# Performance work log

Measured on AMD Instinct MI355X. Metric: run time of the kernel, lower is better.

## Reference

```python
import jax, jax.numpy as jnp
import numpy as np

_BN_EPS = 1e-5
_BN_SCALE = 1.0 / np.sqrt(1.0 + _BN_EPS)  # eval-mode BN with running_mean=0, running_var=1


def _bn(x, g, b):
    # eval-mode BatchNorm1d over channel dim (last axis here)
    return x * (g * _BN_SCALE) + b


def _sa_layer(src_xyz, dst_xyz, cur_i, idx, empty, p_w, p_g, p_b, m_w, m_g, m_b):
    # src_xyz: (N,3), dst_xyz: (M,3), cur_i: (N,D), idx: (M,S) int, empty: (M,) bool
    idx = idx.astype(jnp.int32)
    sp = src_xyz[idx]                       # (M,S,3) neighbor gather
    dp = dst_xyz[:, None, :]                # (M,1,3)
    feat6 = jnp.concatenate([sp - dp, jnp.broadcast_to(dp, sp.shape)], axis=-1)  # (M,S,6)
    off = jax.nn.silu(_bn(jnp.einsum('msc,dc->msd', feat6, p_w), p_g, p_b))      # (M,S,D)
    x = off + cur_i[idx]                    # (M,S,D)
    x = jnp.where(empty[:, None, None], 0.0, x)
    h = jax.nn.relu(_bn(jnp.einsum('msd,hd->msh', x, m_w), m_g, m_b))            # (M,S,H)
    return jnp.max(h, axis=1)               # (M,H) max-pool over neighbors


def reference(src_xyz, src_feats, dst_xyz, idx0, idx1, empty0, empty1,
              fc0_w, fc0_b, p0_w, p0_g, p0_b, m0_w, m0_g, m0_b,
              fc1_w, fc1_b, p1_w, p1_g, p1_b, m1_w, m1_g, m1_b,
              out_w, out_g, out_b):
    cur0 = src_feats @ fc0_w.T + fc0_b      # (N,64) fc_i of layer 0
    cur1 = src_feats @ fc1_w.T + fc1_b      # (N,64) fc_i of layer 1
    f0 = _sa_layer(src_xyz, dst_xyz, cur0, idx0, empty0, p0_w, p0_g, p0_b, m0_w, m0_g, m0_b)
    f1 = _sa_layer(src_xyz, dst_xyz, cur1, idx1, empty1, p1_w, p1_g, p1_b, m1_w, m1_g, m1_b)
    feats = jnp.concatenate([f0, f1], axis=1)                                    # (M,256)
    out = jax.nn.relu(_bn(feats @ out_w.T, out_g, out_b))                        # out_conv (1x1 conv)
    return out                               # (M,256)


def setup_inputs() -> dict:
    key = jax.random.key(0)
    ks = jax.random.split(key, 24)
    N, M, Cin, D, H, S0, S1 = 65536, 16384, 64, 64, 128, 16, 32
    inp = {
        'src_xyz': jax.random.normal(ks[0], (N, 3), jnp.float32) * 20.0,
        'src_feats': jax.random.normal(ks[1], (N, Cin), jnp.float32),
        'dst_xyz': jax.random.normal(ks[2], (M, 3), jnp.float32) * 20.0,
        'idx0': jax.random.randint(ks[3], (M, S0), 0, N, jnp.int32),
        'idx1': jax.random.randint(ks[4], (M, S1), 0, N, jnp.int32),
        'empty0': jax.random.bernoulli(ks[5], 0.05, (M,)),
        'empty1': jax.random.bernoulli(ks[6], 0.05, (M,)),
        'fc0_w': jax.random.normal(ks[7], (D, Cin), jnp.float32) / np.sqrt(Cin),
        'fc0_b': jnp.zeros((D,), jnp.float32),
        'p0_w': jax.random.normal(ks[8], (D, 6), jnp.float32) / np.sqrt(6.0),
        'p0_g': jnp.ones((D,), jnp.float32),
        'p0_b': jnp.zeros((D,), jnp.float32),
        'm0_w': jax.random.normal(ks[9], (H, D), jnp.float32) / np.sqrt(D),
        'm0_g': jnp.ones((H,), jnp.float32),
        'm0_b': jnp.zeros((H,), jnp.float32),
        'fc1_w': jax.random.normal(ks[10], (D, Cin), jnp.float32) / np.sqrt(Cin),
        'fc1_b': jnp.zeros((D,), jnp.float32),
        'p1_w': jax.random.normal(ks[11], (D, 6), jnp.float32) / np.sqrt(6.0),
        'p1_g': jnp.ones((D,), jnp.float32),
        'p1_b': jnp.zeros((D,), jnp.float32),
        'm1_w': jax.random.normal(ks[12], (H, D), jnp.float32) / np.sqrt(D),
        'm1_g': jnp.ones((H,), jnp.float32),
        'm1_b': jnp.zeros((H,), jnp.float32),
        'out_w': jax.random.normal(ks[13], (256, 2 * H), jnp.float32) / np.sqrt(2.0 * H),
        'out_g': jnp.ones((256,), jnp.float32),
        'out_b': jnp.zeros((256,), jnp.float32),
    }
    return inp
```

## Files before the change

### kernel.cpp

```cpp
#include <hip/hip_runtime.h>
#include <hip/hip_bf16.h>

typedef unsigned short ushort_t;
typedef unsigned int uint_t;
typedef __attribute__((ext_vector_type(8))) short v8s;
typedef __attribute__((ext_vector_type(4))) float v4f;

#define BN_SCALE 0.9999950000374997f

__device__ __forceinline__ float bf2f(ushort_t u) {
    union { uint_t i; float f; } v;
    v.i = ((uint_t)u) << 16;
    return v.f;
}
__device__ __forceinline__ ushort_t f2bf(float f) {
    union { uint_t i; float f; } v;
    v.f = f;
    uint_t b = v.i;
    b += 0x7fffu + ((b >> 16) & 1u);
    return (ushort_t)(b >> 16);
}

__device__ __forceinline__ v8s cvt8(const float* __restrict__ p) {
    v8s f;
    #pragma unroll
    for (int j = 0; j < 8; ++j) f[j] = (short)f2bf(p[j]);
    return f;
}

__global__ __launch_bounds__(256) void cur_conv_kernel(
    const float* __restrict__ src_feats,
    const float* __restrict__ fc0_w, const float* __restrict__ fc0_b,
    const float* __restrict__ fc1_w, const float* __restrict__ fc1_b,
    ushort_t* __restrict__ cur0, ushort_t* __restrict__ cur1,
    const float* __restrict__ out_w, ushort_t* __restrict__ out_wb,
    const float* __restrict__ m0_w,  ushort_t* __restrict__ m0_wb,
    const float* __restrict__ m1_w,  ushort_t* __restrict__ m1_wb,
    const int CURB)
{
    if (blockIdx.x >= CURB) {
        const int b = blockIdx.x - CURB;
        const float* src;
        ushort_t* dst;
        int base;
        if (b < 64)      { src = out_w; dst = out_wb; base = b; }
        else if (b < 72) { src = m0_w;  dst = m0_wb;  base = b - 64; }
        else             { src = m1_w;  dst = m1_wb;  base = b - 72; }
        const int i = (base * 256 + threadIdx.x) * 4;
        const v4f v = *(const v4f*)(src + i);
        ushort_t r0 = f2bf(v[0]), r1 = f2bf(v[1]), r2 = f2bf(v[2]), r3 = f2bf(v[3]);
        uint_t lo = (uint_t)r0 | ((uint_t)r1 << 16);
        uint_t hi = (uint_t)r2 | ((uint_t)r3 << 16);
        *(uint2*)(dst + i) = make_uint2(lo, hi);
        return;
    }

    const int tid  = threadIdx.x;
    const int lane = tid & 63;
    const int wid  = tid >> 6;
    const int col  = lane & 15;
    const int quad = lane >> 4;
    const int row0 = blockIdx.x * 64 + wid * 16;

    v8s afrag[2];
    #pragma unroll
    for (int kf = 0; kf < 2; ++kf)
        afrag[kf] = cvt8(src_feats + (size_t)(row0 + col) * 64 + kf * 32 + quad * 8);

    v4f acc[8];
    v8s bfrag[8][2];
    #pragma unroll
    for (int ct = 0; ct < 8; ++ct) {
        const int d = (ct & 3) * 16 + col;
        const float* w = (ct < 4 ? fc0_w : fc1_w) + d * 64;
        const float  b = (ct < 4 ? fc0_b : fc1_b)[d];
        acc[ct] = (v4f){b, b, b, b};
        #pragma unroll
        for (int kf = 0; kf < 2; ++kf)
            bfrag[ct][kf] = cvt8(w + kf * 32 + quad * 8);
    }

    #pragma unroll
    for (int kf = 0; kf < 2; ++kf)
        #pragma unroll
        for (int ct = 0; ct < 8; ++ct)
            acc[ct] = __builtin_amdgcn_mfma_f32_16x16x32_bf16(
                afrag[kf], bfrag[ct][kf], acc[ct], 0, 0, 0);

    #pragma unroll
    for (int ct = 0; ct < 8; ++ct) {
        ushort_t* dst = (ct < 4) ? cur0 : cur1;
        const int d = (ct & 3) * 16 + col;
        #pragma unroll
        for (int r = 0; r < 4; ++r) {
            const int n = row0 + quad * 4 + r;
            dst[(size_t)n * 64 + d] = f2bf(acc[ct][r]);
        }
    }
}

template <int S>
__device__ __forceinline__ void sa_body(
    const int bid,
    const float* __restrict__ src_xyz,
    const float* __restrict__ dst_xyz,
    const int*   __restrict__ idx,
    const int*   __restrict__ empty,
    const float* __restrict__ p_w,
    const float* __restrict__ p_g,
    const float* __restrict__ p_b,
    const ushort_t* __restrict__ m_wb,
    const float* __restrict__ m_g,
    const float* __restrict__ m_b,
    const ushort_t* __restrict__ cur,
    ushort_t*    __restrict__ f01,
    const int layer_off,
    ushort_t* xlds,
    v4f*      flds)
{
    constexpr int PAIRS = 128;
    constexpr int MB = PAIRS / S;
    constexpr int XP = 72;
    constexpr int T  = S / 4;

    const int tid  = threadIdx.x;
    const int lane = tid & 63;
    const int wid  = tid >> 6;
    const int m0   = bid * MB;

    {
        const int p  = tid >> 1;
        const int hf = tid & 1;
        const int m  = m0 + p / S;
        const int i  = idx[(size_t)m * S + (p & (S - 1))];
        const uint_t* crow = (const uint_t*)(cur + (size_t)i * 64) + hf * 16;
        const uint4 c0 = *(const uint4*)(crow + 0);
        const uint4 c1 = *(const uint4*)(crow + 4);
        const uint4 c2 = *(const uint4*)(crow + 8);
        const uint4 c3 = *(const uint4*)(crow + 12);
        uint_t* drow = (uint_t*)(xlds + p * XP) + hf * 16;
        *(uint4*)(drow + 0)  = c0;
        *(uint4*)(drow + 4)  = c1;
        *(uint4*)(drow + 8)  = c2;
        *(uint4*)(drow + 12) = c3;
    }
    if (tid < PAIRS) {
        const int p = tid;
        const int m = m0 + p / S;
        const int i = idx[(size_t)m * S + (p & (S - 1))];
        const float dx = dst_xyz[m * 3 + 0];
        const float dy = dst_xyz[m * 3 + 1];
        const float dz = dst_xyz[m * 3 + 2];
        v4f r;
        r[0] = src_xyz[i * 3 + 0] - dx;
        r[1] = src_xyz[i * 3 + 1] - dy;
        r[2] = src_xyz[i * 3 + 2] - dz;
        r[3] = 0.0f;
        flds[p] = r;
    }

    const int dd = (lane & 31) * 2;
    const int psub = lane >> 5;
    const float pgA = p_g[dd] * BN_SCALE;
    const float pgB = p_g[dd + 1] * BN_SCALE;
    const float pbA = p_b[dd];
    const float pbB = p_b[dd + 1];
    const float pwA0 = p_w[dd * 6 + 0] * pgA;
    const float pwA1 = p_w[dd * 6 + 1] * pgA;
    const float pwA2 = p_w[dd * 6 + 2] * pgA;
    const float pdA0 = p_w[dd * 6 + 3] * pgA;
    const float pdA1 = p_w[dd * 6 + 4] * pgA;
    const float pdA2 = p_w[dd * 6 + 5] * pgA;
    const float pwB0 = p_w[dd * 6 + 6] * pgB;
    const float pwB1 = p_w[dd * 6 + 7] * pgB;
    const float pwB2 = p_w[dd * 6 + 8] * pgB;
    const float pdB0 = p_w[dd * 6 + 9] * pgB;
    const float pdB1 = p_w[dd * 6 + 10] * pgB;
    const float pdB2 = p_w[dd * 6 + 11] * pgB;

    __syncthreads();

    const int tbase = wid * T;
    #pragma unroll
    for (int mi = 0; mi < MB; ++mi) {
        const int m = m0 + mi;
        const float dx = dst_xyz[m * 3 + 0];
        const float dy = dst_xyz[m * 3 + 1];
        const float dz = dst_xyz[m * 3 + 2];
        const int   em = empty[m];
        const float vbA = fmaf(pdA0, dx, fmaf(pdA1, dy, fmaf(pdA2, dz, pbA)));
        const float vbB = fmaf(pdB0, dx, fmaf(pdB1, dy, fmaf(pdB2, dz, pbB)));

        #pragma unroll
        for (int it = 0; it < T / 2; ++it) {
            const int p = mi * S + tbase + it * 2 + psub;
            const v4f r = flds[p];
            const uint_t cu = *(const uint_t*)(xlds + p * XP + dd);
            const float c0 = __uint_as_float(cu << 16);
            const float c1 = __uint_as_float(cu & 0xffff0000u);

            const float v0 = fmaf(pwA0, r[0], fmaf(pwA1, r[1], fmaf(pwA2, r[2], vbA)));
            const float v1 = fmaf(pwB0, r[0], fmaf(pwB1, r[1], fmaf(pwB2, r[2], vbB)));
            const float rc0 = __builtin_amdgcn_rcpf(1.0f + __expf(-v0));
            const float rc1 = __builtin_amdgcn_rcpf(1.0f + __expf(-v1));
            float x0 = fmaf(v0, rc0, c0);
            float x1 = fmaf(v1, rc1, c1);
            x0 = em ? 0.0f : x0;
            x1 = em ? 0.0f : x1;

            float2 f2; f2.x = x0; f2.y = x1;
            union { __hip_bfloat162 h2; uint_t u; } pk;
            pk.h2 = __float22bfloat162_rn(f2);
            *(uint_t*)(xlds + p * XP + dd) = pk.u;
        }
    }

    const int col  = lane & 15;
    const int quad = lane >> 4;
    v8s bfrag[2][2];
    float mgv[2], mbv[2];
    #pragma unroll
    for (int c = 0; c < 2; ++c) {
        const int h = (wid * 2 + c) * 16 + col;
        #pragma unroll
        for (int kf = 0; kf < 2; ++kf)
            bfrag[c][kf] = *(const v8s*)(m_wb + h * 64 + kf * 32 + quad * 8);
        mgv[c] = m_g[h] * BN_SCALE;
        mbv[c] = m_b[h];
    }

    __syncthreads();

    #pragma unroll
    for (int mi = 0; mi < MB; ++mi) {
        const int m = m0 + mi;
        v4f acc[S / 16][2];
        #pragma unroll
        for (int rt = 0; rt < S / 16; ++rt)
            #pragma unroll
            for (int c = 0; c < 2; ++c)
                acc[rt][c] = (v4f)0.0f;

        #pragma unroll
        for (int rt = 0; rt < S / 16; ++rt) {
            #pragma unroll
            for (int kf = 0; kf < 2; ++kf) {
                const v8s afrag = *(const v8s*)(
                    xlds + ((mi * S + rt * 16 + col)) * XP + kf * 32 + quad * 8);
                acc[rt][0] = __builtin_amdgcn_mfma_f32_16x16x32_bf16(
                    afrag, bfrag[0][kf], acc[rt][0], 0, 0, 0);
                acc[rt][1] = __builtin_amdgcn_mfma_f32_16x16x32_bf16(
                    afrag, bfrag[1][kf], acc[rt][1], 0, 0, 0);
            }
        }

        float vmax0 = 0.0f, vmax1 = 0.0f;
        #pragma unroll
        for (int c = 0; c < 2; ++c) {
            float vm = 0.0f;
            #pragma unroll
            for (int rt = 0; rt < S / 16; ++rt)
                #pragma unroll
                for (int r = 0; r < 4; ++r) {
                    const float y = fmaf(acc[rt][c][r], mgv[c], mbv[c]);
                    vm = fmaxf(vm, y);
                }
            vm = fmaxf(vm, __shfl_xor(vm, 16));
            vm = fmaxf(vm, __shfl_xor(vm, 32));
            if (c == 0) vmax0 = vm; else vmax1 = vm;
        }
        if (lane < 32) {
            const int c = lane >> 4;
            const float val = (c == 0) ? vmax0 : vmax1;
            f01[m * 256 + layer_off + (wid * 2 + c) * 16 + (lane & 15)] = f2bf(val);
        }
    }
}

__global__ __launch_bounds__(256, 6) void sa_fused_kernel(
    const float* __restrict__ src_xyz, const float* __restrict__ dst_xyz,
    const int* __restrict__ idx0, const int* __restrict__ empty0,
    const float* __restrict__ p0_w, const float* __restrict__ p0_g, const float* __restrict__ p0_b,
    const ushort_t* __restrict__ m0_wb, const float* __restrict__ m0_g, const float* __restrict__ m0_b,
    const ushort_t* __restrict__ cur0,
    const int* __restrict__ idx1, const int* __restrict__ empty1,
    const float* __restrict__ p1_w, const float* __restrict__ p1_g, const float* __restrict__ p1_b,
    const ushort_t* __restrict__ m1_wb, const float* __restrict__ m1_g, const float* __restrict__ m1_b,
    const ushort_t* __restrict__ cur1,
    ushort_t* __restrict__ f01, const int G32)
{
    __shared__ __align__(16) ushort_t xlds[128 * 72];
    __shared__ v4f      flds[128];

    const int b = blockIdx.x;
    if (b < G32)
        sa_body<32>(b, src_xyz, dst_xyz, idx1, empty1, p1_w, p1_g, p1_b,
                    m1_wb, m1_g, m1_b, cur1, f01, 128, xlds, flds);
    else
        sa_body<16>(b - G32, src_xyz, dst_xyz, idx0, empty0, p0_w, p0_g, p0_b,
                    m0_wb, m0_g, m0_b, cur0, f01, 0, xlds, flds);
}

__global__ __launch_bounds__(256) void out_kernel(
    const ushort_t* __restrict__ f01,
    const ushort_t* __restrict__ out_wb,
    const float*    __restrict__ out_g,
    const float*    __restrict__ out_b,
    float*          __restrict__ out)
{
    const int tid  = threadIdx.x;
    const int lane = tid & 63;
    const int wid  = tid >> 6;
    const int col  = lane & 15;
    const int quad = lane >> 4;
    const int m0   = blockIdx.x * 16;

    v8s afrag[8];
    #pragma unroll
    for (int kf = 0; kf < 8; ++kf)
        afrag[kf] = *(const v8s*)(f01 + (size_t)(m0 + col) * 256 + kf * 32 + quad * 8);

    v4f acc[4];
    #pragma unroll
    for (int c = 0; c < 4; ++c) acc[c] = (v4f)0.0f;

    #pragma unroll
    for (int kf = 0; kf < 8; ++kf) {
        #pragma unroll
        for (int c = 0; c < 4; ++c) {
            const int n = (wid * 4 + c) * 16 + col;
            const v8s b = *(const v8s*)(out_wb + (size_t)n * 256 + kf * 32 + quad * 8);
            acc[c] = __builtin_amdgcn_mfma_f32_16x16x32_bf16(afrag[kf], b, acc[c], 0, 0, 0);
        }
    }

    #pragma unroll
    for (int c = 0; c < 4; ++c) {
        const int n  = (wid * 4 + c) * 16 + col;
        const float og = out_g[n] * BN_SCALE;
        const float ob = out_b[n];
        #pragma unroll
        for (int r = 0; r < 4; ++r) {
            float y = fmaf(acc[c][r], og, ob);
            y = fmaxf(y, 0.0f);
            out[(size_t)(m0 + quad * 4 + r) * 256 + n] = y;
        }
    }
}

extern "C" void kernel_launch(void* const* d_in, const int* in_sizes, int n_in,
                              void* d_out, int out_size, void* d_ws, size_t ws_size,
                              hipStream_t stream)
{
    const float* src_xyz   = (const float*)d_in[0];
    const float* src_feats = (const float*)d_in[1];
    const float* dst_xyz   = (const float*)d_in[2];
    const int*   idx0      = (const int*)d_in[3];
    const int*   idx1      = (const int*)d_in[4];
    const int*   empty0    = (const int*)d_in[5];
    const int*   empty1    = (const int*)d_in[6];
    const float* fc0_w     = (const float*)d_in[7];
    const float* fc0_b     = (const float*)d_in[8];
    const float* p0_w      = (const float*)d_in[9];
    const float* p0_g      = (const float*)d_in[10];
    const float* p0_b      = (const float*)d_in[11];
    const float* m0_w      = (const float*)d_in[12];
    const float* m0_g      = (const float*)d_in[13];
    const float* m0_b      = (const float*)d_in[14];
    const float* fc1_w     = (const float*)d_in[15];
    const float* fc1_b     = (const float*)d_in[16];
    const float* p1_w      = (const float*)d_in[17];
    const float* p1_g      = (const float*)d_in[18];
    const float* p1_b      = (const float*)d_in[19];
    const float* m1_w      = (const float*)d_in[20];
    const float* m1_g      = (const float*)d_in[21];
    const float* m1_b      = (const float*)d_in[22];
    const float* out_w     = (const float*)d_in[23];
    const float* out_g     = (const float*)d_in[24];
    const float* out_b     = (const float*)d_in[25];

    const int N = in_sizes[0] / 3;
    const int M = in_sizes[2] / 3;

    ushort_t* cur0   = (ushort_t*)d_ws;
    ushort_t* cur1   = cur0 + (size_t)N * 64;
    ushort_t* f01    = cur1 + (size_t)N * 64;
    ushort_t* out_wb = f01 + (size_t)M * 256;
    ushort_t* m0_wb  = out_wb + 256 * 256;
    ushort_t* m1_wb  = m0_wb + 128 * 64;

    const int G32 = M / 4;
    const int G16 = M / 8;
    const int CURB = N / 64;

    cur_conv_kernel<<<CURB + 80, 256, 0, stream>>>(
        src_feats, fc0_w, fc0_b, fc1_w, fc1_b, cur0, cur1,
        out_w, out_wb, m0_w, m0_wb, m1_w, m1_wb, CURB);
    sa_fused_kernel<<<G32 + G16, 256, 0, stream>>>(
        src_xyz, dst_xyz,
        idx0, empty0, p0_w, p0_g, p0_b, m0_wb, m0_g, m0_b, cur0,
        idx1, empty1, p1_w, p1_g, p1_b, m1_wb, m1_g, m1_b, cur1,
        f01, G32);
    out_kernel<<<M / 16, 256, 0, stream>>>(f01, out_wb, out_g, out_b,
                                           (float*)d_out);
}
```

Measured before the change: 195.4 us.

## Pre-convert fc weights to bf16, pack position FMAs, skip empty groups

Adds a small kernel that converts the fc weights to bf16 once, so the per-block cur conversion loads bf16 fragments directly instead of converting floats in every block. In the SA kernel, relative coordinates are stored duplicated in LDS so the positional linear can use packed two-wide FMAs. Fully empty neighbourhoods are handled by writing zeros and skipping the silu math. The SA kernel's occupancy hint drops from 6 to 4 waves, which allows more registers per thread but may hide less latency. The trade-offs are an extra kernel launch and more LDS traffic from the duplicated coordinates.

```diff
diff --git a/kernel.cpp b/kernel.cpp
--- a/kernel.cpp
+++ b/kernel.cpp
@@ -5,6 +5,7 @@
 typedef unsigned int uint_t;
 typedef __attribute__((ext_vector_type(8))) short v8s;
 typedef __attribute__((ext_vector_type(4))) float v4f;
+typedef __attribute__((ext_vector_type(2))) float v2f;
 
 #define BN_SCALE 0.9999950000374997f
 
@@ -28,10 +29,33 @@
     return f;
 }
 
+__device__ __forceinline__ v2f pkfma(v2f a, v2f b, v2f c) {
+#if __has_builtin(__builtin_elementwise_fma)
+    return __builtin_elementwise_fma(a, b, c);
+#else
+    v2f d; d[0] = fmaf(a[0], b[0], c[0]); d[1] = fmaf(a[1], b[1], c[1]); return d;
+#endif
+}
+
+__global__ __launch_bounds__(256) void fcconv_kernel(
+    const float* __restrict__ fc0_w, ushort_t* __restrict__ fc0_wb,
+    const float* __restrict__ fc1_w, ushort_t* __restrict__ fc1_wb)
+{
+    const int b = blockIdx.x;
+    const float* src = (b < 4) ? fc0_w : fc1_w;
+    ushort_t*    dst = (b < 4) ? fc0_wb : fc1_wb;
+    const int i = ((b & 3) * 256 + threadIdx.x) * 4;
+    const v4f v = *(const v4f*)(src + i);
+    ushort_t r0 = f2bf(v[0]), r1 = f2bf(v[1]), r2 = f2bf(v[2]), r3 = f2bf(v[3]);
+    uint_t lo = (uint_t)r0 | ((uint_t)r1 << 16);
+    uint_t hi = (uint_t)r2 | ((uint_t)r3 << 16);
+    *(uint2*)(dst + i) = make_uint2(lo, hi);
+}
+
 __global__ __launch_bounds__(256) void cur_conv_kernel(
     const float* __restrict__ src_feats,
-    const float* __restrict__ fc0_w, const float* __restrict__ fc0_b,
-    const float* __restrict__ fc1_w, const float* __restrict__ fc1_b,
+    const ushort_t* __restrict__ fc0_wb, const float* __restrict__ fc0_b,
+    const ushort_t* __restrict__ fc1_wb, const float* __restrict__ fc1_b,
     ushort_t* __restrict__ cur0, ushort_t* __restrict__ cur1,
     const float* __restrict__ out_w, ushort_t* __restrict__ out_wb,
     const float* __restrict__ m0_w,  ushort_t* __restrict__ m0_wb,
@@ -72,12 +96,12 @@
     #pragma unroll
     for (int ct = 0; ct < 8; ++ct) {
         const int d = (ct & 3) * 16 + col;
-        const float* w = (ct < 4 ? fc0_w : fc1_w) + d * 64;
+        const ushort_t* w = (ct < 4 ? fc0_wb : fc1_wb) + d * 64;
         const float  b = (ct < 4 ? fc0_b : fc1_b)[d];
         acc[ct] = (v4f){b, b, b, b};
         #pragma unroll
         for (int kf = 0; kf < 2; ++kf)
-            bfrag[ct][kf] = cvt8(w + kf * 32 + quad * 8);
+            bfrag[ct][kf] = *(const v8s*)(w + kf * 32 + quad * 8);
     }
 
     #pragma unroll
@@ -116,7 +140,7 @@
     ushort_t*    __restrict__ f01,
     const int layer_off,
     ushort_t* xlds,
-    v4f*      flds)
+    float*    fdup)
 {
     constexpr int PAIRS = 128;
     constexpr int MB = PAIRS / S;
@@ -148,15 +172,16 @@
         const int p = tid;
         const int m = m0 + p / S;
         const int i = idx[(size_t)m * S + (p & (S - 1))];
-        const float dx = dst_xyz[m * 3 + 0];
-        const float dy = dst_xyz[m * 3 + 1];
-        const float dz = dst_xyz[m * 3 + 2];
-        v4f r;
-        r[0] = src_xyz[i * 3 + 0] - dx;
-        r[1] = src_xyz[i * 3 + 1] - dy;
-        r[2] = src_xyz[i * 3 + 2] - dz;
-        r[3] = 0.0f;
-        flds[p] = r;
+        const float rx = src_xyz[i * 3 + 0] - dst_xyz[m * 3 + 0];
+        const float ry = src_xyz[i * 3 + 1] - dst_xyz[m * 3 + 1];
+        const float rz = src_xyz[i * 3 + 2] - dst_xyz[m * 3 + 2];
+        float* fd = fdup + p * 6;
+        v2f a0; a0[0] = rx; a0[1] = rx;
+        v2f a1; a1[0] = ry; a1[1] = ry;
+        v2f a2; a2[0] = rz; a2[1] = rz;
+        *(v2f*)(fd + 0) = a0;
+        *(v2f*)(fd + 2) = a1;
+        *(v2f*)(fd + 4) = a2;
     }
 
     const int dd = (lane & 31) * 2;
@@ -165,16 +190,13 @@
     const float pgB = p_g[dd + 1] * BN_SCALE;
     const float pbA = p_b[dd];
     const float pbB = p_b[dd + 1];
-    const float pwA0 = p_w[dd * 6 + 0] * pgA;
-    const float pwA1 = p_w[dd * 6 + 1] * pgA;
-    const float pwA2 = p_w[dd * 6 + 2] * pgA;
+    v2f pw0; pw0[0] = p_w[dd * 6 + 0] * pgA;  pw0[1] = p_w[dd * 6 + 6]  * pgB;
+    v2f pw1; pw1[0] = p_w[dd * 6 + 1] * pgA;  pw1[1] = p_w[dd * 6 + 7]  * pgB;
+    v2f pw2; pw2[0] = p_w[dd * 6 + 2] * pgA;  pw2[1] = p_w[dd * 6 + 8]  * pgB;
     const float pdA0 = p_w[dd * 6 + 3] * pgA;
     const float pdA1 = p_w[dd * 6 + 4] * pgA;
     const float pdA2 = p_w[dd * 6 + 5] * pgA;
-    const float pwB0 = p_w[dd * 6 + 6] * pgB;
-    const float pwB1 = p_w[dd * 6 + 7] * pgB;
-    const float pwB2 = p_w[dd * 6 + 8] * pgB;
-    const float pdB0 = p_w[dd * 6 + 9] * pgB;
+    const float pdB0 = p_w[dd * 6 + 9]  * pgB;
     const float pdB1 = p_w[dd * 6 + 10] * pgB;
     const float pdB2 = p_w[dd * 6 + 11] * pgB;
 
@@ -184,34 +206,43 @@
     #pragma unroll
     for (int mi = 0; mi < MB; ++mi) {
         const int m = m0 + mi;
-        const float dx = dst_xyz[m * 3 + 0];
-        const float dy = dst_xyz[m * 3 + 1];
-        const float dz = dst_xyz[m * 3 + 2];
-        const int   em = empty[m];
-        const float vbA = fmaf(pdA0, dx, fmaf(pdA1, dy, fmaf(pdA2, dz, pbA)));
-        const float vbB = fmaf(pdB0, dx, fmaf(pdB1, dy, fmaf(pdB2, dz, pbB)));
-
-        #pragma unroll
-        for (int it = 0; it < T / 2; ++it) {
-            const int p = mi * S + tbase + it * 2 + psub;
-            const v4f r = flds[p];
-            const uint_t cu = *(const uint_t*)(xlds + p * XP + dd);
-            const float c0 = __uint_as_float(cu << 16);
-            const float c1 = __uint_as_float(cu & 0xffff0000u);
-
-            const float v0 = fmaf(pwA0, r[0], fmaf(pwA1, r[1], fmaf(pwA2, r[2], vbA)));
-            const float v1 = fmaf(pwB0, r[0], fmaf(pwB1, r[1], fmaf(pwB2, r[2], vbB)));
-            const float rc0 = __builtin_amdgcn_rcpf(1.0f + __expf(-v0));
-            const float rc1 = __builtin_amdgcn_rcpf(1.0f + __expf(-v1));
-            float x0 = fmaf(v0, rc0, c0);
-            float x1 = fmaf(v1, rc1, c1);
-            x0 = em ? 0.0f : x0;
-            x1 = em ? 0.0f : x1;
-
-            float2 f2; f2.x = x0; f2.y = x1;
-            union { __hip_bfloat162 h2; uint_t u; } pk;
-            pk.h2 = __float22bfloat162_rn(f2);
-            *(uint_t*)(xlds + p * XP + dd) = pk.u;
+        const int em = empty[m];
+        if (em) {
+            #pragma unroll
+            for (int it = 0; it < T / 2; ++it) {
+                const int p = mi * S + tbase + it * 2 + psub;
+                *(uint_t*)(xlds + p * XP + dd) = 0u;
+            }
+        } else {
+            const float dx = dst_xyz[m * 3 + 0];
+            const float dy = dst_xyz[m * 3 + 1];
+            const float dz = dst_xyz[m * 3 + 2];
+            const float vbA = fmaf(pdA0, dx, fmaf(pdA1, dy, fmaf(pdA2, dz, pbA)));
+            const float vbB = fmaf(pdB0, dx, fmaf(pdB1, dy, fmaf(pdB2, dz, pbB)));
+            v2f vb; vb[0] = vbA; vb[1] = vbB;
+
+            #pragma unroll
+            for (int it = 0; it < T / 2; ++it) {
+                const int p = mi * S + tbase + it * 2 + psub;
+                const float* fd = fdup + p * 6;
+                const v2f rr0 = *(const v2f*)(fd + 0);
+                const v2f rr1 = *(const v2f*)(fd + 2);
+                const v2f rr2 = *(const v2f*)(fd + 4);
+                const uint_t cu = *(const uint_t*)(xlds + p * XP + dd);
+
+                const v2f v = pkfma(pw0, rr0, pkfma(pw1, rr1, pkfma(pw2, rr2, vb)));
+                const float rc0 = __builtin_amdgcn_rcpf(1.0f + __expf(-v[0]));
+                const float rc1 = __builtin_amdgcn_rcpf(1.0f + __expf(-v[1]));
+                const float c0 = __uint_as_float(cu << 16);
+                const float c1 = __uint_as_float(cu & 0xffff0000u);
+                const float x0 = fmaf(v[0], rc0, c0);
+                const float x1 = fmaf(v[1], rc1, c1);
+
+                float2 f2; f2.x = x0; f2.y = x1;
+                union { __hip_bfloat162 h2; uint_t u; } pk;
+                pk.h2 = __float22bfloat162_rn(f2);
+                *(uint_t*)(xlds + p * XP + dd) = pk.u;
+            }
         }
     }
 
@@ -277,7 +308,7 @@
     }
 }
 
-__global__ __launch_bounds__(256, 6) void sa_fused_kernel(
+__global__ __launch_bounds__(256, 4) void sa_fused_kernel(
     const float* __restrict__ src_xyz, const float* __restrict__ dst_xyz,
     const int* __restrict__ idx0, const int* __restrict__ empty0,
     const float* __restrict__ p0_w, const float* __restrict__ p0_g, const float* __restrict__ p0_b,
@@ -290,15 +321,15 @@
     ushort_t* __restrict__ f01, const int G32)
 {
     __shared__ __align__(16) ushort_t xlds[128 * 72];
-    __shared__ v4f      flds[128];
+    __shared__ __align__(16) float    fdup[128 * 6];
 
     const int b = blockIdx.x;
     if (b < G32)
         sa_body<32>(b, src_xyz, dst_xyz, idx1, empty1, p1_w, p1_g, p1_b,
-                    m1_wb, m1_g, m1_b, cur1, f01, 128, xlds, flds);
+                    m1_wb, m1_g, m1_b, cur1, f01, 128, xlds, fdup);
     else
         sa_body<16>(b - G32, src_xyz, dst_xyz, idx0, empty0, p0_w, p0_g, p0_b,
-                    m0_wb, m0_g, m0_b, cur0, f01, 0, xlds, flds);
+                    m0_wb, m0_g, m0_b, cur0, f01, 0, xlds, fdup);
 }
 
 __global__ __launch_bounds__(256) void out_kernel(
@@ -388,13 +419,16 @@
     ushort_t* out_wb = f01 + (size_t)M * 256;
     ushort_t* m0_wb  = out_wb + 256 * 256;
     ushort_t* m1_wb  = m0_wb + 128 * 64;
+    ushort_t* fc0_wb = m1_wb + 128 * 64;
+    ushort_t* fc1_wb = fc0_wb + 64 * 64;
 
     const int G32 = M / 4;
     const int G16 = M / 8;
     const int CURB = N / 64;
 
+    fcconv_kernel<<<8, 256, 0, stream>>>(fc0_w, fc0_wb, fc1_w, fc1_wb);
     cur_conv_kernel<<<CURB + 80, 256, 0, stream>>>(
-        src_feats, fc0_w, fc0_b, fc1_w, fc1_b, cur0, cur1,
+        src_feats, fc0_wb, fc0_b, fc1_wb, fc1_b, cur0, cur1,
         out_w, out_wb, m0_w, m0_wb, m1_w, m1_wb, CURB);
     sa_fused_kernel<<<G32 + G16, 256, 0, stream>>>(
         src_xyz, dst_xyz,
```

Result: no change. 192.9 us (-1.3%).
